# Kernel optimization log

Hardware: AMD Instinct MI355X
Metric: run time of the kernel (lower is better)

The kernel has to match this reference:

```python
import jax, jax.numpy as jnp
import numpy as np

N_NODES = 100000
D = 256
N_TYPES = 4
E1 = 300000
E2 = 300000


def setup_inputs() -> dict:
    key = jax.random.key(0)
    ks = jax.random.split(key, 9)
    x = jax.random.normal(ks[0], (N_NODES, D), dtype=jnp.float32)
    hyperedge_index_s1 = jax.random.randint(ks[1], (2, E1 * 1), 0, N_NODES, dtype=jnp.int32)
    hyperedge_type_s1 = jax.random.randint(ks[2], (E1,), 0, N_TYPES, dtype=jnp.int32)
    hyperedge_index_s2 = jax.random.randint(ks[3], (2, E2 * 2), 0, N_NODES, dtype=jnp.int32)
    hyperedge_type_s2 = jax.random.randint(ks[4], (E2,), 0, N_TYPES, dtype=jnp.int32)
    # xavier_normal init for A: std = sqrt(2 / (fan_in + fan_out))
    A_s1 = jax.random.normal(ks[5], (N_TYPES, 1 * D, D), dtype=jnp.float32) * np.sqrt(2.0 / (D + D)).astype(np.float32)
    A_s2 = jax.random.normal(ks[6], (N_TYPES, 2 * D, D), dtype=jnp.float32) * np.sqrt(2.0 / (2 * D + D)).astype(np.float32)
    lim = 1.0 / np.sqrt(D)
    W_c = jax.random.uniform(ks[7], (D, D), minval=-lim, maxval=lim, dtype=jnp.float32)
    b_c = jax.random.uniform(ks[8], (D,), minval=-lim, maxval=lim, dtype=jnp.float32)
    return dict(x=x,
                hyperedge_index_s1=hyperedge_index_s1, hyperedge_type_s1=hyperedge_type_s1,
                hyperedge_index_s2=hyperedge_index_s2, hyperedge_type_s2=hyperedge_type_s2,
                A_s1=A_s1, A_s2=A_s2, W_c=W_c, b_c=b_c)


def _shape_agg(x, A, idx, etype, shape, n_nodes):
    """Per-hyperedge-shape gather -> per-type matmul -> normalize -> scatter-add."""
    d = x.shape[1]
    e = etype.shape[0]
    # concat the `shape` source node features per hyperedge: [E, shape*d]
    src = x[idx[0]].reshape(e, shape * d)
    # first target slot per hyperedge: [E]
    dst = idx[1].reshape(e, shape)[:, 0]
    agg = jnp.zeros((n_nodes, d), dtype=x.dtype)
    for t in range(A.shape[0]):  # small fixed number of edge types
        mask = etype == t
        tmp = src @ A[t]  # [E, d]
        # per-destination count within this (shape, type) group == torch.unique counts
        counts = jax.ops.segment_sum(mask.astype(x.dtype), dst, num_segments=n_nodes)
        norm = jnp.where(mask, 1.0 / jnp.maximum(counts[dst], 1.0), 0.0)
        agg = agg.at[dst].add(norm[:, None] * tmp)
    return agg


def reference(x, hyperedge_index_s1, hyperedge_type_s1,
              hyperedge_index_s2, hyperedge_type_s2,
              A_s1, A_s2, W_c, b_c):
    n = x.shape[0]
    agg = _shape_agg(x, A_s1, hyperedge_index_s1, hyperedge_type_s1, 1, n)
    agg = agg + _shape_agg(x, A_s2, hyperedge_index_s2, hyperedge_type_s2, 2, n)
    return x @ W_c.T + b_c + agg
```

## Files before the change

kernel.cpp:

```cpp
#include <hip/hip_runtime.h>
#include <stdint.h>

#define N_NODES 100000
#define D 256
#define NT 4

typedef float f32x4 __attribute__((ext_vector_type(4)));
typedef __bf16 bf16x8 __attribute__((ext_vector_type(8)));
typedef unsigned int uint32x4 __attribute__((ext_vector_type(4)));
typedef unsigned int uint32x2 __attribute__((ext_vector_type(2)));

__device__ __forceinline__ unsigned short f2bf(float f) {
    unsigned u = __float_as_uint(f);
    u += 0x7FFF + ((u >> 16) & 1);
    return (unsigned short)(u >> 16);
}

__device__ __forceinline__ void gload_lds16(const void* g, void* lds) {
    __builtin_amdgcn_global_load_lds(
        (const __attribute__((address_space(1))) unsigned int*)g,
        (__attribute__((address_space(3))) unsigned int*)lds, 16, 0, 0);
}


template<int SHAPE>
__global__ void k_count(const int* __restrict__ idx, const int* __restrict__ etype,
                        int E, int* __restrict__ counts) {
    int e = blockIdx.x * 256 + threadIdx.x;
    if (e >= E) return;
    int t = etype[e];
    int dst = idx[(size_t)SHAPE * E + (size_t)SHAPE * e];
    atomicAdd(&counts[t * N_NODES + dst], 1);
}


__global__ __launch_bounds__(256) void k_scan1(const int* __restrict__ in, int n,
        int* __restrict__ outv, int* __restrict__ bsums) {
    __shared__ int s[256];
    int tid = threadIdx.x;
    int i = blockIdx.x * 1024 + tid * 4;
    int v0 = 0, v1 = 0, v2 = 0, v3 = 0;
    if (i + 3 < n) {
        int4 v = *(const int4*)(in + i);
        v0 = v.x; v1 = v.y; v2 = v.z; v3 = v.w;
    } else {
        if (i     < n) v0 = in[i];
        if (i + 1 < n) v1 = in[i + 1];
        if (i + 2 < n) v2 = in[i + 2];
        if (i + 3 < n) v3 = in[i + 3];
    }
    int tsum = v0 + v1 + v2 + v3;
    s[tid] = tsum; __syncthreads();
    for (int off = 1; off < 256; off <<= 1) {
        int t = (tid >= off) ? s[tid - off] : 0;
        __syncthreads();
        s[tid] += t;
        __syncthreads();
    }
    int excl = s[tid] - tsum;
    if (tid == 255) bsums[blockIdx.x] = s[255];
    int o0 = excl, o1 = o0 + v0, o2 = o1 + v1, o3 = o2 + v2;
    if (i + 3 < n) {
        *(int4*)(outv + i) = make_int4(o0, o1, o2, o3);
    } else {
        if (i     < n) outv[i]     = o0;
        if (i + 1 < n) outv[i + 1] = o1;
        if (i + 2 < n) outv[i + 2] = o2;
        if (i + 3 < n) outv[i + 3] = o3;
    }
}

__global__ void k_scan2(int* __restrict__ bsums, int nb) {
    __shared__ int s[512];
    int t = threadIdx.x;
    int v = (t < nb) ? bsums[t] : 0;
    s[t] = v; __syncthreads();
    for (int off = 1; off < 512; off <<= 1) {
        int u = (t >= off) ? s[t - off] : 0;
        __syncthreads();
        s[t] += u;
        __syncthreads();
    }
    if (t < nb) bsums[t] = s[t] - v;
}

__global__ __launch_bounds__(256) void k_scan3(int* __restrict__ cellofs,
        int* __restrict__ cellcur, const int* __restrict__ bsums, int n) {
    int i = blockIdx.x * 1024 + threadIdx.x * 4;
    int add = bsums[blockIdx.x];
    if (i + 3 < n) {
        int4 v = *(int4*)(cellofs + i);
        v.x += add; v.y += add; v.z += add; v.w += add;
        *(int4*)(cellofs + i) = v;
        *(int4*)(cellcur + i) = v;
    } else {
        for (int k = 0; k < 4; ++k)
            if (i + k < n) { int v = cellofs[i + k] + add; cellofs[i + k] = v; cellcur[i + k] = v; }
    }
}


template<int SHAPE>
__global__ void k_place(const int* __restrict__ idx, const int* __restrict__ etype, int E,
                        int* __restrict__ cellcur, int* __restrict__ bucket) {
    int e = blockIdx.x * 256 + threadIdx.x;
    if (e >= E) return;
    int t = etype[e];
    int dst = idx[(size_t)SHAPE * E + (size_t)SHAPE * e];
    int pos = atomicAdd(&cellcur[t * N_NODES + dst], 1);
    bucket[pos] = e;
}


__global__ __launch_bounds__(256) void k_cvt(const float* __restrict__ in,
        unsigned short* __restrict__ ob, int n8) {
    int i = blockIdx.x * 256 + threadIdx.x;
    if (i >= n8) return;
    const float4* p = (const float4*)in + (size_t)i * 2;
    float4 v0 = p[0], v1 = p[1];
    union { unsigned short us[8]; uint4 u4; } o;
    o.us[0] = f2bf(v0.x); o.us[1] = f2bf(v0.y); o.us[2] = f2bf(v0.z); o.us[3] = f2bf(v0.w);
    o.us[4] = f2bf(v1.x); o.us[5] = f2bf(v1.y); o.us[6] = f2bf(v1.z); o.us[7] = f2bf(v1.w);
    *(uint4*)(ob + (size_t)i * 8) = o.u4;
}


__global__ void k_cvt_At(const float* __restrict__ A, unsigned short* __restrict__ AT, int K) {
    __shared__ float tl[32][33];
    const float* Ab = A + (size_t)blockIdx.z * K * D;
    unsigned short* Ob = AT + (size_t)blockIdx.z * D * K;
    int k0 = blockIdx.x * 32, j0 = blockIdx.y * 32;
    int lx = threadIdx.x, ly = threadIdx.y;
    for (int yy = ly; yy < 32; yy += 8)
        tl[yy][lx] = Ab[(size_t)(k0 + yy) * D + j0 + lx];
    __syncthreads();
    for (int yy = ly; yy < 32; yy += 8)
        Ob[(size_t)(j0 + yy) * K + k0 + lx] = f2bf(tl[lx][yy]);
}


__global__ __launch_bounds__(256) void k_init_mfma(const unsigned short* __restrict__ xb,
        const unsigned short* __restrict__ Wb, const float* __restrict__ bias,
        float* __restrict__ out, int n) {
    __shared__ __align__(16) char xs[64 * 128];
    int row0 = blockIdx.x * 64;
    int tid = threadIdx.x;
    int lane = tid & 63, w = tid >> 6;
    int l15 = lane & 15, l4 = lane >> 4;
    f32x4 acc[4][4];
    #pragma unroll
    for (int m = 0; m < 4; ++m)
        #pragma unroll
        for (int nn = 0; nn < 4; ++nn) acc[m][nn] = (f32x4)0.f;

    for (int kk = 0; kk < D; kk += 64) {
        #pragma unroll
        for (int it = 0; it < 2; ++it) {
            int f = it * 256 + tid;
            int r = f >> 3, q0 = f & 7;
            int q = q0 ^ (r & 7);
            int gr = row0 + r; if (gr >= n) gr = n - 1;
            gload_lds16(xb + (size_t)gr * D + kk + q * 8, xs + f * 16);
        }
        bf16x8 bfr[2][4];
        #pragma unroll
        for (int ks = 0; ks < 2; ++ks)
            #pragma unroll
            for (int nn = 0; nn < 4; ++nn) {
                int j = w * 64 + nn * 16 + l15;
                int k = kk + ks * 32 + l4 * 8;
                bfr[ks][nn] = *(const bf16x8*)(Wb + (size_t)j * D + k);
            }
        __syncthreads();
        #pragma unroll
        for (int ks = 0; ks < 2; ++ks)
            #pragma unroll
            for (int m = 0; m < 4; ++m) {
                int R = m * 16 + l15;
                int C = ks * 4 + l4;
                bf16x8 a = *(const bf16x8*)(xs + R * 128 + ((C ^ (R & 7)) << 4));
                #pragma unroll
                for (int nn = 0; nn < 4; ++nn)
                    acc[m][nn] = __builtin_amdgcn_mfma_f32_16x16x32_bf16(
                        a, bfr[ks][nn], acc[m][nn], 0, 0, 0);
            }
        __syncthreads();
    }
    #pragma unroll
    for (int m = 0; m < 4; ++m)
        #pragma unroll
        for (int nn = 0; nn < 4; ++nn) {
            int col = w * 64 + nn * 16 + l15;
            float bv = bias[col];
            #pragma unroll
            for (int r = 0; r < 4; ++r) {
                int row = row0 + m * 16 + l4 * 4 + r;
                if (row < n) out[(size_t)row * D + col] = acc[m][nn][r] + bv;
            }
        }
}


template<int SHAPE, int SCR>
__global__ __launch_bounds__(256) void k_edge_mfma(const unsigned short* __restrict__ xb,
        const int* __restrict__ idx, const unsigned short* __restrict__ AT,
        float* __restrict__ out, unsigned short* __restrict__ eo, int E,
        const int* __restrict__ counts, const int* __restrict__ cellofs,
        const int* __restrict__ bucket) {
    constexpr int K = SHAPE * 256;
    __shared__ __align__(16) char xs[64 * 128];
    __shared__ unsigned short re[32][264];
    __shared__ int srcS[SHAPE][64];
    __shared__ int dstS[64];
    __shared__ float normS[64];

    int t = blockIdx.y;
    int offs_t = cellofs[t * N_NODES];
    int end_t = (t == NT - 1) ? E : cellofs[(t + 1) * N_NODES];
    int cnt = end_t - offs_t;
    int tile = blockIdx.x * 64;
    if (tile >= cnt) return;
    int nE = min(64, cnt - tile);
    int base = offs_t + tile;
    int tid = threadIdx.x;

    if (tid < 64) {
        bool valid = tid < nE;
        int e = bucket[base + (valid ? tid : 0)];
        int dst = idx[(size_t)SHAPE * E + (size_t)SHAPE * e];
        dstS[tid] = dst;
        int c = counts[t * N_NODES + dst];
        normS[tid] = valid ? 1.0f / (float)(c > 1 ? c : 1) : 0.0f;
        srcS[0][tid] = idx[SHAPE * e];
        if (SHAPE == 2) srcS[SHAPE - 1][tid] = idx[SHAPE * e + SHAPE - 1];
    }
    __syncthreads();

    const unsigned short* Bt = AT + (size_t)t * D * K;
    int lane = tid & 63, w = tid >> 6;
    int l15 = lane & 15, l4 = lane >> 4;
    f32x4 acc[4][4];
    #pragma unroll
    for (int m = 0; m < 4; ++m)
        #pragma unroll
        for (int nn = 0; nn < 4; ++nn) acc[m][nn] = (f32x4)0.f;

    for (int kk = 0; kk < K; kk += 64) {
        #pragma unroll
        for (int it = 0; it < 2; ++it) {
            int f = it * 256 + tid;
            int r = f >> 3, q0 = f & 7;
            int q = q0 ^ (r & 7);
            int node = srcS[SHAPE == 2 ? (kk >> 8) : 0][r];
            int col = (kk & 255) + q * 8;
            gload_lds16(xb + (size_t)node * D + col, xs + f * 16);
        }
        bf16x8 bfr[2][4];
        #pragma unroll
        for (int ks = 0; ks < 2; ++ks)
            #pragma unroll
            for (int nn = 0; nn < 4; ++nn) {
                int j = w * 64 + nn * 16 + l15;
                int k = kk + ks * 32 + l4 * 8;
                bfr[ks][nn] = *(const bf16x8*)(Bt + (size_t)j * K + k);
            }
        __syncthreads();
        #pragma unroll
        for (int ks = 0; ks < 2; ++ks)
            #pragma unroll
            for (int m = 0; m < 4; ++m) {
                int R = m * 16 + l15;
                int C = ks * 4 + l4;
                bf16x8 a = *(const bf16x8*)(xs + R * 128 + ((C ^ (R & 7)) << 4));
                #pragma unroll
                for (int nn = 0; nn < 4; ++nn)
                    acc[m][nn] = __builtin_amdgcn_mfma_f32_16x16x32_bf16(
                        a, bfr[ks][nn], acc[m][nn], 0, 0, 0);
            }
        __syncthreads();
    }

    if constexpr (SCR) {
        #pragma unroll
        for (int half = 0; half < 2; ++half) {
            if (half) __syncthreads();
            #pragma unroll
            for (int mi = 0; mi < 2; ++mi) {
                int m = half * 2 + mi;
                #pragma unroll
                for (int r = 0; r < 4; ++r) {
                    int rr = m * 16 + l4 * 4 + r;
                    float nm = normS[rr];
                    int rl = rr - half * 32;
                    #pragma unroll
                    for (int nn = 0; nn < 4; ++nn) {
                        int col = w * 64 + nn * 16 + l15;
                        re[rl][col] = f2bf(nm * acc[m][nn][r]);
                    }
                }
            }
            __syncthreads();
            #pragma unroll
            for (int it = 0; it < 4; ++it) {
                int f = it * 256 + tid;
                int row = f >> 5, seg = f & 31;
                int grow = half * 32 + row;
                if (grow < nE) {
                    uint32x4 v = *(const uint32x4*)&re[row][seg * 8];
                    __builtin_nontemporal_store(v,
                        (uint32x4*)(eo + (size_t)(base + grow) * D + seg * 8));
                }
            }
        }
    } else {
        #pragma unroll
        for (int m = 0; m < 4; ++m)
            #pragma unroll
            for (int r = 0; r < 4; ++r) {
                int rr = m * 16 + l4 * 4 + r;
                if (rr < nE) {
                    float nm = normS[rr];
                    size_t ob = (size_t)dstS[rr] * D;
                    #pragma unroll
                    for (int nn = 0; nn < 4; ++nn) {
                        int col = w * 64 + nn * 16 + l15;
                        atomicAdd(&out[ob + col], nm * acc[m][nn][r]);
                    }
                }
            }
    }
}


__device__ __forceinline__ void acc_runs(const unsigned short* __restrict__ eo,
        const int* __restrict__ counts, const int* __restrict__ cellofs,
        int dst, int lane, float& a0, float& a1, float& a2, float& a3, int& tot) {
    #pragma unroll
    for (int t = 0; t < NT; ++t) {
        int start = cellofs[t * N_NODES + dst];
        int c = counts[t * N_NODES + dst];
        tot += c;
        for (int i = 0; i < c; ++i) {
            const uint32x2* row = (const uint32x2*)(eo + (size_t)(start + i) * D + lane * 4);
            uint32x2 v = __builtin_nontemporal_load(row);
            a0 += __uint_as_float(v.x << 16);
            a1 += __uint_as_float(v.x & 0xFFFF0000u);
            a2 += __uint_as_float(v.y << 16);
            a3 += __uint_as_float(v.y & 0xFFFF0000u);
        }
    }
}

__global__ __launch_bounds__(256) void k_reduce_one(const unsigned short* __restrict__ eo,
        const int* __restrict__ counts, const int* __restrict__ cellofs,
        float* __restrict__ out) {
    int wv = threadIdx.x >> 6, lane = threadIdx.x & 63;
    int dst = blockIdx.x * 4 + wv;
    if (dst >= N_NODES) return;
    float a0 = 0.f, a1 = 0.f, a2 = 0.f, a3 = 0.f;
    int tot = 0;
    acc_runs(eo, counts, cellofs, dst, lane, a0, a1, a2, a3, tot);
    if (tot) {
        float4* o = (float4*)&out[(size_t)dst * D + lane * 4];
        float4 cur = *o;
        cur.x += a0; cur.y += a1; cur.z += a2; cur.w += a3;
        *o = cur;
    }
}

__global__ __launch_bounds__(256) void k_reduce_two(
        const unsigned short* __restrict__ eo1, const int* __restrict__ c1, const int* __restrict__ o1,
        const unsigned short* __restrict__ eo2, const int* __restrict__ c2, const int* __restrict__ o2,
        float* __restrict__ out) {
    int wv = threadIdx.x >> 6, lane = threadIdx.x & 63;
    int dst = blockIdx.x * 4 + wv;
    if (dst >= N_NODES) return;
    float a0 = 0.f, a1 = 0.f, a2 = 0.f, a3 = 0.f;
    int tot = 0;
    acc_runs(eo1, c1, o1, dst, lane, a0, a1, a2, a3, tot);
    acc_runs(eo2, c2, o2, dst, lane, a0, a1, a2, a3, tot);
    if (tot) {
        float4* o = (float4*)&out[(size_t)dst * D + lane * 4];
        float4 cur = *o;
        cur.x += a0; cur.y += a1; cur.z += a2; cur.w += a3;
        *o = cur;
    }
}


extern "C" void kernel_launch(void* const* d_in, const int* in_sizes, int n_in,
                              void* d_out, int out_size, void* d_ws, size_t ws_size,
                              hipStream_t stream) {
    const float* x  = (const float*)d_in[0];
    const int* idx1 = (const int*)d_in[1];
    const int* ty1  = (const int*)d_in[2];
    const int* idx2 = (const int*)d_in[3];
    const int* ty2  = (const int*)d_in[4];
    const float* A1 = (const float*)d_in[5];
    const float* A2 = (const float*)d_in[6];
    const float* W  = (const float*)d_in[7];
    const float* b  = (const float*)d_in[8];
    float* out = (float*)d_out;

    int E1 = in_sizes[2];
    int E2 = in_sizes[4];
    int maxE = E1 > E2 ? E1 : E2;
    const int NCELL = NT * N_NODES;
    const int NB = (NCELL + 1023) / 1024;
    const int NRB = (N_NODES + 3) / 4;

    char* p = (char*)d_ws;
    unsigned short* xb  = (unsigned short*)p; p += (size_t)N_NODES * D * 2;
    unsigned short* Wb  = (unsigned short*)p; p += (size_t)D * D * 2;
    unsigned short* A1T = (unsigned short*)p; p += (size_t)NT * D * 256 * 2;
    unsigned short* A2T = (unsigned short*)p; p += (size_t)NT * D * 512 * 2;
    int* counts1 = (int*)p; p += (size_t)NCELL * 4;
    int* cellofs1= (int*)p; p += (size_t)NCELL * 4;
    int* counts2 = (int*)p; p += (size_t)NCELL * 4;
    int* cellofs2= (int*)p; p += (size_t)NCELL * 4;
    int* cellcur = (int*)p; p += (size_t)NCELL * 4;
    int* bsums   = (int*)p; p += 512 * 4;
    int* bucket  = (int*)p; p += (size_t)maxE * 4;
    unsigned short* eo1 = (unsigned short*)p; p += (size_t)maxE * D * 2;
    size_t need1 = (size_t)(p - (char*)d_ws);
    unsigned short* eo2 = (unsigned short*)p; p += (size_t)maxE * D * 2;
    size_t need2 = (size_t)(p - (char*)d_ws);
    int mode = (need2 <= ws_size) ? 2 : (need1 <= ws_size) ? 1 : 0;

    k_cvt<<<(N_NODES * D / 8 + 255) / 256, 256, 0, stream>>>(x, xb, N_NODES * D / 8);
    k_cvt<<<(D * D / 8 + 255) / 256, 256, 0, stream>>>(W, Wb, D * D / 8);
    k_cvt_At<<<dim3(256 / 32, D / 32, NT), dim3(32, 8), 0, stream>>>(A1, A1T, 256);
    k_cvt_At<<<dim3(512 / 32, D / 32, NT), dim3(32, 8), 0, stream>>>(A2, A2T, 512);

    k_init_mfma<<<(N_NODES + 63) / 64, 256, 0, stream>>>(xb, Wb, b, out, N_NODES);

    hipMemsetAsync(counts1, 0, (size_t)NCELL * sizeof(int), stream);
    k_count<1><<<(E1 + 255) / 256, 256, 0, stream>>>(idx1, ty1, E1, counts1);
    k_scan1<<<NB, 256, 0, stream>>>(counts1, NCELL, cellofs1, bsums);
    k_scan2<<<1, 512, 0, stream>>>(bsums, NB);
    k_scan3<<<NB, 256, 0, stream>>>(cellofs1, cellcur, bsums, NCELL);
    k_place<1><<<(E1 + 255) / 256, 256, 0, stream>>>(idx1, ty1, E1, cellcur, bucket);
    if (mode) {
        k_edge_mfma<1, 1><<<dim3((E1 + 63) / 64, NT), 256, 0, stream>>>(
            xb, idx1, A1T, out, eo1, E1, counts1, cellofs1, bucket);
        if (mode == 1)
            k_reduce_one<<<NRB, 256, 0, stream>>>(eo1, counts1, cellofs1, out);
    } else {
        k_edge_mfma<1, 0><<<dim3((E1 + 63) / 64, NT), 256, 0, stream>>>(
            xb, idx1, A1T, out, nullptr, E1, counts1, cellofs1, bucket);
    }

    hipMemsetAsync(counts2, 0, (size_t)NCELL * sizeof(int), stream);
    k_count<2><<<(E2 + 255) / 256, 256, 0, stream>>>(idx2, ty2, E2, counts2);
    k_scan1<<<NB, 256, 0, stream>>>(counts2, NCELL, cellofs2, bsums);
    k_scan2<<<1, 512, 0, stream>>>(bsums, NB);
    k_scan3<<<NB, 256, 0, stream>>>(cellofs2, cellcur, bsums, NCELL);
    k_place<2><<<(E2 + 255) / 256, 256, 0, stream>>>(idx2, ty2, E2, cellcur, bucket);
    if (mode) {
        unsigned short* eoS2 = (mode == 2) ? eo2 : eo1;
        k_edge_mfma<2, 1><<<dim3((E2 + 63) / 64, NT), 256, 0, stream>>>(
            xb, idx2, A2T, out, eoS2, E2, counts2, cellofs2, bucket);
        if (mode == 2)
            k_reduce_two<<<NRB, 256, 0, stream>>>(eo1, counts1, cellofs1,
                                                  eo2, counts2, cellofs2, out);
        else
            k_reduce_one<<<NRB, 256, 0, stream>>>(eo1, counts2, cellofs2, out);
    } else {
        k_edge_mfma<2, 0><<<dim3((E2 + 63) / 64, NT), 256, 0, stream>>>(
            xb, idx2, A2T, out, nullptr, E2, counts2, cellofs2, bucket);
    }
}
```

Measured before the change: 607.7 us.

## Alias edge-kernel LDS buffers and cap launch bounds to raise occupancy

The edge MFMA kernel now shares one LDS buffer between the gather tile and the epilogue staging area. The staging area shrinks to 16 rows, so the epilogue writes out in four quarters instead of two halves. Launch bounds request 4 blocks per multiprocessor, and the nontemporal stores become plain stores. The aim is lower LDS use and register pressure so more blocks are resident, at the cost of extra barriers in the epilogue and possible register spilling.

```diff
diff --git a/kernel.cpp b/kernel.cpp
--- a/kernel.cpp
+++ b/kernel.cpp
@@ -202,14 +202,13 @@
 
 
 template<int SHAPE, int SCR>
-__global__ __launch_bounds__(256) void k_edge_mfma(const unsigned short* __restrict__ xb,
+__global__ __launch_bounds__(256, 4) void k_edge_mfma(const unsigned short* __restrict__ xb,
         const int* __restrict__ idx, const unsigned short* __restrict__ AT,
         float* __restrict__ out, unsigned short* __restrict__ eo, int E,
         const int* __restrict__ counts, const int* __restrict__ cellofs,
         const int* __restrict__ bucket) {
     constexpr int K = SHAPE * 256;
-    __shared__ __align__(16) char xs[64 * 128];
-    __shared__ unsigned short re[32][264];
+    __shared__ __align__(16) char smem[16 * 264 * 2];
     __shared__ int srcS[SHAPE][64];
     __shared__ int dstS[64];
     __shared__ float normS[64];
@@ -253,7 +252,7 @@
             int q = q0 ^ (r & 7);
             int node = srcS[SHAPE == 2 ? (kk >> 8) : 0][r];
             int col = (kk & 255) + q * 8;
-            gload_lds16(xb + (size_t)node * D + col, xs + f * 16);
+            gload_lds16(xb + (size_t)node * D + col, smem + f * 16);
         }
         bf16x8 bfr[2][4];
         #pragma unroll
@@ -271,7 +270,7 @@
             for (int m = 0; m < 4; ++m) {
                 int R = m * 16 + l15;
                 int C = ks * 4 + l4;
-                bf16x8 a = *(const bf16x8*)(xs + R * 128 + ((C ^ (R & 7)) << 4));
+                bf16x8 a = *(const bf16x8*)(smem + R * 128 + ((C ^ (R & 7)) << 4));
                 #pragma unroll
                 for (int nn = 0; nn < 4; ++nn)
                     acc[m][nn] = __builtin_amdgcn_mfma_f32_16x16x32_bf16(
@@ -281,34 +280,29 @@
     }
 
     if constexpr (SCR) {
-        #pragma unroll
-        for (int half = 0; half < 2; ++half) {
-            if (half) __syncthreads();
-            #pragma unroll
-            for (int mi = 0; mi < 2; ++mi) {
-                int m = half * 2 + mi;
+        unsigned short (*re)[264] = (unsigned short (*)[264])smem;
+        #pragma unroll
+        for (int q = 0; q < 4; ++q) {
+            if (q) __syncthreads();
+            #pragma unroll
+            for (int r = 0; r < 4; ++r) {
+                int rl = l4 * 4 + r;
+                float nm = normS[q * 16 + rl];
                 #pragma unroll
-                for (int r = 0; r < 4; ++r) {
-                    int rr = m * 16 + l4 * 4 + r;
-                    float nm = normS[rr];
-                    int rl = rr - half * 32;
-                    #pragma unroll
-                    for (int nn = 0; nn < 4; ++nn) {
-                        int col = w * 64 + nn * 16 + l15;
-                        re[rl][col] = f2bf(nm * acc[m][nn][r]);
-                    }
+                for (int nn = 0; nn < 4; ++nn) {
+                    int col = w * 64 + nn * 16 + l15;
+                    re[rl][col] = f2bf(nm * acc[q][nn][r]);
                 }
             }
             __syncthreads();
             #pragma unroll
-            for (int it = 0; it < 4; ++it) {
+            for (int it = 0; it < 2; ++it) {
                 int f = it * 256 + tid;
                 int row = f >> 5, seg = f & 31;
-                int grow = half * 32 + row;
+                int grow = q * 16 + row;
                 if (grow < nE) {
                     uint32x4 v = *(const uint32x4*)&re[row][seg * 8];
-                    __builtin_nontemporal_store(v,
-                        (uint32x4*)(eo + (size_t)(base + grow) * D + seg * 8));
+                    *(uint32x4*)(eo + (size_t)(base + grow) * D + seg * 8) = v;
                 }
             }
         }
```

Result: faster. 588.4 us (-3.2%).
